# Performance work log

Measured on AMD Instinct MI355X. Metric: run time of the kernel, lower is better.

The kernel has to match this reference:

```python
import jax, jax.numpy as jnp
import numpy as np
import math

B, S, D_MODEL, H, D_LATENT = 2, 2048, 2048, 16, 512
D_HEAD = D_MODEL // H


def setup_inputs() -> dict:
    key = jax.random.key(0)
    ks = jax.random.split(key, 6)
    s = lambda fan: 1.0 / math.sqrt(fan)
    return {
        "x": jax.random.normal(ks[0], (B, S, D_MODEL), dtype=jnp.float32),
        "W_q": jax.random.normal(ks[1], (D_MODEL, D_MODEL), dtype=jnp.float32) * s(D_MODEL),
        "W_down_kv": jax.random.normal(ks[2], (D_LATENT, D_MODEL), dtype=jnp.float32) * s(D_MODEL),
        "W_up_k": jax.random.normal(ks[3], (H, D_HEAD, D_LATENT), dtype=jnp.float32) * s(D_LATENT),
        "W_up_v": jax.random.normal(ks[4], (H, D_HEAD, D_LATENT), dtype=jnp.float32) * s(D_LATENT),
        "W_o": jax.random.normal(ks[5], (D_MODEL, D_MODEL), dtype=jnp.float32) * s(D_MODEL),
    }


def reference(x, W_q, W_down_kv, W_up_k, W_up_v, W_o):
    b, s_len, d_model = x.shape
    # Q: (B, H, S, Dh)
    Q = (x @ W_q.T).reshape(b, s_len, H, D_HEAD).transpose(0, 2, 1, 3)
    # latent KV: (B, S, d_latent)
    C_kv = x @ W_down_kv.T
    # per-head up-projections fused into one einsum: (B, H, S, Dh)
    K = jnp.einsum("bsl,hdl->bhsd", C_kv, W_up_k)
    V = jnp.einsum("bsl,hdl->bhsd", C_kv, W_up_v)
    scores = jnp.einsum("bhsd,bhtd->bhst", Q, K) / math.sqrt(D_HEAD)
    attn = jax.nn.softmax(scores, axis=-1)  # dropout p=0 / eval -> identity
    out = jnp.einsum("bhst,bhtd->bhsd", attn, V)
    out = out.transpose(0, 2, 1, 3).reshape(b, s_len, H * D_HEAD)
    return out @ W_o.T
```

## Files before the change

kernel.cpp:

```cpp
#include <hip/hip_runtime.h>
#include <hip/hip_bf16.h>

typedef __hip_bfloat16 bf16;
typedef __attribute__((ext_vector_type(8))) short short8v;
typedef __attribute__((ext_vector_type(4))) short short4v;
typedef __attribute__((ext_vector_type(4))) float f32x4;
typedef __attribute__((ext_vector_type(16))) float f32x16;
typedef __attribute__((ext_vector_type(4))) unsigned int uint4v;
typedef unsigned int u32;

#define MFMA_16x16x32(a, b, c) __builtin_amdgcn_mfma_f32_16x16x32_bf16((a), (b), (c), 0, 0, 0)
#define MFMA_32x32x16(a, b, c) __builtin_amdgcn_mfma_f32_32x32x16_bf16((a), (b), (c), 0, 0, 0)

constexpr int Bc = 2, Sc = 2048, DMc = 2048, Hc = 16, DLc = 512, DHc = 128;

__device__ __forceinline__ void gload_lds16(const bf16* g, void* lds) {
  __builtin_amdgcn_global_load_lds(
      (const __attribute__((address_space(1))) void*)g,
      (__attribute__((address_space(3))) void*)lds, 16, 0, 0);
}

__device__ __forceinline__ unsigned short bf16bits(float f) {
  return __builtin_bit_cast(unsigned short, __float2bfloat16(f));
}

struct CvtArgs {
  const float* src[6];
  bf16* dst[6];
  unsigned int cum[6];
  unsigned int total4;
};

__global__ __launch_bounds__(256) void cvt_all_kernel(CvtArgs a)
{
  unsigned int i = blockIdx.x * 256 + threadIdx.x;
  const unsigned int stride = gridDim.x * 256;
  for (; i < a.total4; i += stride) {
    int s = 0;
#pragma unroll
    for (int k = 1; k < 6; ++k) s += (i >= a.cum[k]) ? 1 : 0;
    unsigned int off = (i - a.cum[s]) * 4;
    float4 v = *(const float4*)(a.src[s] + off);
    short4v p;
    p[0] = (short)bf16bits(v.x);
    p[1] = (short)bf16bits(v.y);
    p[2] = (short)bf16bits(v.z);
    p[3] = (short)bf16bits(v.w);
    *(short4v*)(a.dst[s] + off) = p;
  }
}

template<int EPI>
__device__ __forceinline__ void gemm_tile_128(
    const bf16* __restrict__ A, const bf16* __restrict__ BT, void* __restrict__ Cv,
    int K, int ldc, int row0, int col0, bf16* As, bf16* Bs)
{
  const int tid = threadIdx.x;
  const int lane = tid & 63, wid = tid >> 6;
  const int wr = wid >> 1, wc = wid & 1;

  f32x4 acc[4][4] = {};

  const int srow = tid >> 2;
  const int scol = (tid & 3) * 8;
  const bf16* Ag = A + (size_t)(row0 + srow) * K + scol;
  const bf16* Bg = BT + (size_t)(col0 + srow) * K + scol;
  char* AsW = (char*)As + wid * 1024;
  char* BsW = (char*)Bs + wid * 1024;

  const int fr = lane & 15, fk = (lane >> 4) * 8;
  const bf16* aRd = As + (wr * 64 + fr) * 32 + fk;
  const bf16* bRd = Bs + (wc * 64 + fr) * 32 + fk;

  for (int k0 = 0; k0 < K; k0 += 32) {
    gload_lds16(Ag, AsW);
    gload_lds16(Ag + (size_t)64 * K, AsW + 4096);
    gload_lds16(Bg, BsW);
    gload_lds16(Bg + (size_t)64 * K, BsW + 4096);
    Ag += 32; Bg += 32;
    __syncthreads();
    short8v a[4], b[4];
#pragma unroll
    for (int m = 0; m < 4; ++m) a[m] = *(const short8v*)(aRd + m * 16 * 32);
#pragma unroll
    for (int n = 0; n < 4; ++n) b[n] = *(const short8v*)(bRd + n * 16 * 32);
#pragma unroll
    for (int m = 0; m < 4; ++m)
#pragma unroll
      for (int n = 0; n < 4; ++n)
        acc[m][n] = MFMA_16x16x32(a[m], b[n], acc[m][n]);
    __syncthreads();
  }

  const int crow = (lane >> 4) * 4, ccol = lane & 15;
  if (EPI == 0) {
    bf16* C = (bf16*)Cv;
#pragma unroll
    for (int m = 0; m < 4; ++m)
#pragma unroll
      for (int n = 0; n < 4; ++n) {
        bf16* Cp = C + (size_t)(row0 + wr * 64 + m * 16 + crow) * ldc
                     + col0 + wc * 64 + n * 16 + ccol;
#pragma unroll
        for (int r = 0; r < 4; ++r)
          Cp[(size_t)r * ldc] = __float2bfloat16(acc[m][n][r]);
      }
  } else if (EPI == 1) {
    bf16* C = (bf16*)Cv;
#pragma unroll
    for (int m = 0; m < 4; ++m)
#pragma unroll
      for (int n = 0; n < 4; ++n) {
        short4v pk;
#pragma unroll
        for (int r = 0; r < 4; ++r)
          pk[r] = (short)bf16bits(acc[m][n][r]);
        bf16* Cp = C + (size_t)(col0 + wc * 64 + n * 16 + ccol) * ldc
                     + row0 + wr * 64 + m * 16 + crow;
        *(short4v*)Cp = pk;
      }
  } else {
    float* C = (float*)Cv;
#pragma unroll
    for (int m = 0; m < 4; ++m)
#pragma unroll
      for (int n = 0; n < 4; ++n) {
        float* Cp = C + (size_t)(row0 + wr * 64 + m * 16 + crow) * ldc
                      + col0 + wc * 64 + n * 16 + ccol;
#pragma unroll
        for (int r = 0; r < 4; ++r)
          Cp[(size_t)r * ldc] = acc[m][n][r];
      }
  }
}

__device__ __forceinline__ int2 xcd_remap(int nx, int ny) {
  int flat = blockIdx.x + nx * blockIdx.y;
  int chunk = (nx * ny) >> 3;
  int role = (flat & 7) * chunk + (flat >> 3);
  return make_int2(role % nx, role / nx);
}

template<int EPI>
__global__ __launch_bounds__(256) void gemm_bt_kernel(
    const bf16* __restrict__ A, const bf16* __restrict__ BT, void* __restrict__ C,
    int K, int N)
{
  __shared__ bf16 As[128 * 32];
  __shared__ bf16 Bs[128 * 32];
  int2 bb = xcd_remap(gridDim.x, gridDim.y);
  gemm_tile_128<EPI>(A, BT, C, K, N, bb.y * 128, bb.x * 128, As, Bs);
}

__global__ __launch_bounds__(256) void qkv_gemm_kernel(
    const bf16* __restrict__ xb, const bf16* __restrict__ Wqb,
    const bf16* __restrict__ Wdkvb, bf16* __restrict__ Qb, bf16* __restrict__ Ck)
{
  __shared__ bf16 As[128 * 32];
  __shared__ bf16 Bs[128 * 32];
  int2 bb = xcd_remap(20, 32);
  const int bx = bb.x, row0 = bb.y * 128;
  if (bx < 16)
    gemm_tile_128<0>(xb, Wqb, Qb, DMc, DMc, row0, bx * 128, As, Bs);
  else
    gemm_tile_128<0>(xb, Wdkvb, Ck, DMc, DLc, row0, (bx - 16) * 128, As, Bs);
}

__global__ __launch_bounds__(256) void up_gemm_kernel(
    const bf16* __restrict__ Ck, const bf16* __restrict__ Wukb,
    const bf16* __restrict__ Wuvb, bf16* __restrict__ Kcat, bf16* __restrict__ VTcat)
{
  __shared__ bf16 As[128 * 32];
  __shared__ bf16 Bs[128 * 32];
  int2 bb = xcd_remap(32, 32);
  const int bx = bb.x, row0 = bb.y * 128;
  if (bx < 16)
    gemm_tile_128<0>(Ck, Wukb, Kcat, DLc, DMc, row0, bx * 128, As, Bs);
  else
    gemm_tile_128<1>(Ck, Wuvb, VTcat, DLc, Bc * Sc, row0, (bx - 16) * 128, As, Bs);
}

constexpr int KVB = 64;
constexpr int NTT = Sc / KVB;
constexpr int VSTR = Bc * Sc;

__global__ __launch_bounds__(256, 2) void mla_attn_kernel(
    const bf16* __restrict__ Q, const bf16* __restrict__ Kcat,
    const bf16* __restrict__ VTcat, bf16* __restrict__ O)
{
  __shared__ bf16 Ks[2][KVB * 128];
  __shared__ bf16 Vs[2][64 * 128];

  const int tid = threadIdx.x, lane = tid & 63, wid = tid >> 6;
  const int l31 = lane & 31, hi = lane >> 5;

  const int flat = blockIdx.x + 16 * (blockIdx.y + 16 * blockIdx.z);
  const int role = (flat & 7) * 64 + (flat >> 3);
  const int qb = role & 15, h = (role >> 4) & 15, b = role >> 8;
  const int q0 = qb * 128 + wid * 32;

  const bf16* Qp = Q + (size_t)(b * Sc + q0 + l31) * DMc + h * DHc + hi * 8;
  short8v qf[8];
#pragma unroll
  for (int kk = 0; kk < 8; ++kk) qf[kk] = *(const short8v*)(Qp + kk * 16);

  const bf16* Kb = Kcat + (size_t)b * Sc * DMc + h * DHc;
  const bf16* Vb = VTcat + (size_t)(h * DHc) * VSTR + b * Sc;

  const int srow = wid * 4 + (lane >> 4);
  const int scolB = (lane & 15) * 16;
  const int swzK0 = ((srow & 7) << 4) ^ (((srow >> 3) & 1) << 6);
  const bf16* kpE = Kb + (size_t)srow * DMc + (((scolB ^ swzK0) & 255) >> 1);
  const bf16* kpO = Kb + (size_t)srow * DMc + ((((scolB ^ swzK0) ^ 128) & 255) >> 1);
  const int swzV0 = ((srow & 7) << 4) ^ (((srow >> 3) & 1) << 7);
  const int vcp = scolB ^ swzV0;
  const bf16* vp = Vb + (size_t)(2 * srow + (vcp >> 7)) * VSTR + ((vcp & 127) >> 1);

  auto STAGE = [&](int buf, int t0) {
    char* kd = (char*)(&Ks[buf][0]) + wid * 1024;
    gload_lds16(kpE + (size_t)t0 * DMc, kd);
    gload_lds16(kpO + (size_t)(t0 + 16) * DMc, kd + 4096);
    gload_lds16(kpE + (size_t)(t0 + 32) * DMc, kd + 8192);
    gload_lds16(kpO + (size_t)(t0 + 48) * DMc, kd + 12288);
    char* vd = (char*)(&Vs[buf][0]) + wid * 1024;
    const bf16* v0 = vp + t0;
    gload_lds16(v0, vd);
    gload_lds16(v0 + (size_t)32 * VSTR, vd + 4096);
    gload_lds16(v0 + (size_t)64 * VSTR, vd + 8192);
    gload_lds16(v0 + (size_t)96 * VSTR, vd + 12288);
  };

  const int swzR = ((l31 & 7) << 4) ^ (((l31 >> 3) & 1) << 6) ^ (((l31 >> 4) & 1) << 7);
  const int swzVR = (((l31 >> 1) & 7) << 4) ^ (((l31 >> 4) & 1) << 7);

  f32x16 oacc[4] = {};
  float m_r = -1e30f, l_r = 0.f, msc = 0.f;
  const float SCL2 = 0.12751650f;
  const float THRraw = 47.0f;

  STAGE(0, 0);
  int cur = 0;

  for (int it = 0; it < NTT; ++it) {
    asm volatile("s_waitcnt vmcnt(0)" ::: "memory");
    __builtin_amdgcn_s_barrier();
    asm volatile("" ::: "memory");
    if (it + 1 < NTT) STAGE(cur ^ 1, (it + 1) * KVB);
    asm volatile("" ::: "memory");

    f32x16 s0 = {}, s1 = {};
    const char* Kc = (const char*)(&Ks[cur][0]);
    __builtin_amdgcn_s_setprio(1);
#pragma unroll
    for (int kk = 0; kk < 8; ++kk) {
      const int cb = (kk * 32 + hi * 16) ^ swzR;
      short8v k0 = *(const short8v*)(Kc + l31 * 256 + cb);
      short8v k1 = *(const short8v*)(Kc + (32 + l31) * 256 + cb);
      s0 = MFMA_32x32x16(k0, qf[kk], s0);
      s1 = MFMA_32x32x16(k1, qf[kk], s1);
    }
    __builtin_amdgcn_s_setprio(0);

    float pm = s0[0];
#pragma unroll
    for (int i = 1; i < 16; ++i) pm = fmaxf(pm, s0[i]);
#pragma unroll
    for (int i = 0; i < 16; ++i) pm = fmaxf(pm, s1[i]);

    if (!__all(pm - m_r <= THRraw)) {
      float red = fmaxf(pm, __shfl_xor(pm, 32, 64));
      float mnew = fmaxf(m_r, red);
      float c = exp2f((m_r - mnew) * SCL2);
      m_r = mnew;
      msc = mnew * SCL2;
      l_r *= c;
#pragma unroll
      for (int db = 0; db < 4; ++db) oacc[db] *= c;
    }

    short8v pf[4];
#pragma unroll
    for (int tt = 0; tt < 2; ++tt) {
      const f32x16& s = tt ? s1 : s0;
#pragma unroll
      for (int half = 0; half < 2; ++half) {
        float e0 = exp2f(__builtin_fmaf(s[half * 8 + 0], SCL2, -msc));
        float e1 = exp2f(__builtin_fmaf(s[half * 8 + 1], SCL2, -msc));
        float e2 = exp2f(__builtin_fmaf(s[half * 8 + 2], SCL2, -msc));
        float e3 = exp2f(__builtin_fmaf(s[half * 8 + 3], SCL2, -msc));
        float e4 = exp2f(__builtin_fmaf(s[half * 8 + 4], SCL2, -msc));
        float e5 = exp2f(__builtin_fmaf(s[half * 8 + 5], SCL2, -msc));
        float e6 = exp2f(__builtin_fmaf(s[half * 8 + 6], SCL2, -msc));
        float e7 = exp2f(__builtin_fmaf(s[half * 8 + 7], SCL2, -msc));
        l_r += ((e0 + e1) + (e2 + e3)) + ((e4 + e5) + (e6 + e7));
        u32 cA, cB, cC, cD;
        asm("v_cvt_pk_bf16_f32 %0, %1, %2" : "=v"(cA) : "v"(e0), "v"(e1));
        asm("v_cvt_pk_bf16_f32 %0, %1, %2" : "=v"(cB) : "v"(e2), "v"(e3));
        asm("v_cvt_pk_bf16_f32 %0, %1, %2" : "=v"(cC) : "v"(e4), "v"(e5));
        asm("v_cvt_pk_bf16_f32 %0, %1, %2" : "=v"(cD) : "v"(e6), "v"(e7));
        asm volatile("v_permlane32_swap_b32 %0, %1" : "+v"(cA), "+v"(cC));
        asm volatile("v_permlane32_swap_b32 %0, %1" : "+v"(cB), "+v"(cD));
        uint4v w;
        w[0] = cA; w[1] = cB; w[2] = cC; w[3] = cD;
        pf[tt * 2 + half] = __builtin_bit_cast(short8v, w);
      }
    }

    const char* Vc = (const char*)(&Vs[cur][0]);
    __builtin_amdgcn_s_setprio(1);
#pragma unroll
    for (int db = 0; db < 4; ++db) {
      const int vrow = (db * 16 + (l31 >> 1)) * 256;
#pragma unroll
      for (int ts = 0; ts < 4; ++ts) {
        const int cb = ((l31 & 1) * 128 + ts * 32 + hi * 16) ^ swzVR;
        short8v vf = *(const short8v*)(Vc + vrow + cb);
        oacc[db] = MFMA_32x32x16(vf, pf[ts], oacc[db]);
      }
    }
    __builtin_amdgcn_s_setprio(0);

    cur ^= 1;
  }

  float l = l_r + __shfl_xor(l_r, 32, 64);
  float inv = 1.f / l;
  bf16* Op = O + (size_t)(b * Sc + q0 + l31) * DMc + h * DHc + hi * 4;
#pragma unroll
  for (int db = 0; db < 4; ++db) {
#pragma unroll
    for (int rq = 0; rq < 4; ++rq) {
      short4v pk;
#pragma unroll
      for (int r = 0; r < 4; ++r)
        pk[r] = (short)bf16bits(oacc[db][rq * 4 + r] * inv);
      *(short4v*)(Op + db * 32 + rq * 8) = pk;
    }
  }
}

extern "C" void kernel_launch(void* const* d_in, const int* in_sizes, int n_in,
                              void* d_out, int out_size, void* d_ws, size_t ws_size,
                              hipStream_t stream)
{
  const float* x    = (const float*)d_in[0];
  const float* Wq   = (const float*)d_in[1];
  const float* Wdkv = (const float*)d_in[2];
  const float* Wuk  = (const float*)d_in[3];
  const float* Wuv  = (const float*)d_in[4];
  const float* Wo   = (const float*)d_in[5];
  float* out = (float*)d_out;

  char* ws = (char*)d_ws;
  bf16* Qb    = (bf16*)(ws + 0);
  bf16* Kcat  = (bf16*)(ws + 16777216);
  bf16* VTcat = (bf16*)(ws + 33554432);
  bf16* xb    = (bf16*)(ws + 50331648);
  bf16* AO    = (bf16*)(ws + 50331648);
  bf16* Ck    = (bf16*)(ws + 67108864);
  bf16* Wqb   = (bf16*)(ws + 71303168);
  bf16* Wdkvb = (bf16*)(ws + 79691776);
  bf16* Wukb  = (bf16*)(ws + 81788928);
  bf16* Wuvb  = (bf16*)(ws + 83886080);
  bf16* Wob   = (bf16*)(ws + 85983232);

  dim3 blk(256, 1, 1);

  CvtArgs ca;
  ca.src[0] = x;    ca.dst[0] = xb;
  ca.src[1] = Wq;   ca.dst[1] = Wqb;
  ca.src[2] = Wdkv; ca.dst[2] = Wdkvb;
  ca.src[3] = Wuk;  ca.dst[3] = Wukb;
  ca.src[4] = Wuv;  ca.dst[4] = Wuvb;
  ca.src[5] = Wo;   ca.dst[5] = Wob;
  unsigned int n4[6] = { (unsigned)(Bc * Sc * DMc / 4), (unsigned)(DMc * DMc / 4),
                         (unsigned)(DLc * DMc / 4),     (unsigned)(Hc * DHc * DLc / 4),
                         (unsigned)(Hc * DHc * DLc / 4),(unsigned)(DMc * DMc / 4) };
  unsigned int acc = 0;
  for (int i = 0; i < 6; ++i) { ca.cum[i] = acc; acc += n4[i]; }
  ca.total4 = acc;
  cvt_all_kernel<<<2048, blk, 0, stream>>>(ca);

  qkv_gemm_kernel<<<dim3(20, (Bc * Sc) / 128), blk, 0, stream>>>(xb, Wqb, Wdkvb, Qb, Ck);

  up_gemm_kernel<<<dim3(32, (Bc * Sc) / 128), blk, 0, stream>>>(Ck, Wukb, Wuvb, Kcat, VTcat);

  mla_attn_kernel<<<dim3(Sc / 128, Hc, Bc), dim3(256, 1, 1), 0, stream>>>(
      Qb, Kcat, VTcat, AO);

  gemm_bt_kernel<2><<<dim3(DMc / 128, (Bc * Sc) / 128), blk, 0, stream>>>(AO, Wob, out, DMc, DMc);
}
```

Measured before the change: 239.8 us.

## Replace 128x128 GEMM tiles with double-buffered swizzled 256x256 tiles

```diff
diff --git a/kernel.cpp b/kernel.cpp
--- a/kernel.cpp
+++ b/kernel.cpp
@@ -50,57 +50,103 @@
   }
 }
 
+#define GPHASE(bufv, KK, MH)                                                \
+  do {                                                                      \
+    const char* ap_ = aR + (bufv) * 32768 + (KK) * 8192 + (MH) * 4096;      \
+    const char* bp_ = bR + (bufv) * 32768 + (KK) * 8192;                    \
+    short8v af_[4], bf_[4];                                                 \
+    _Pragma("unroll")                                                       \
+    for (int m4 = 0; m4 < 4; ++m4)                                          \
+      af_[m4] = *(const short8v*)(ap_ + m4 * 1024);                         \
+    _Pragma("unroll")                                                       \
+    for (int n = 0; n < 4; ++n)                                             \
+      bf_[n] = *(const short8v*)(bp_ + n * 1024);                           \
+    __builtin_amdgcn_s_setprio(1);                                          \
+    _Pragma("unroll")                                                       \
+    for (int m4 = 0; m4 < 4; ++m4)                                          \
+      _Pragma("unroll")                                                     \
+      for (int n = 0; n < 4; ++n)                                           \
+        acc[(MH) * 4 + m4][n] =                                             \
+            MFMA_16x16x32(af_[m4], bf_[n], acc[(MH) * 4 + m4][n]);          \
+    __builtin_amdgcn_s_setprio(0);                                          \
+  } while (0)
+
 template<int EPI>
-__device__ __forceinline__ void gemm_tile_128(
+__device__ __forceinline__ void gemm_tile_256(
     const bf16* __restrict__ A, const bf16* __restrict__ BT, void* __restrict__ Cv,
-    int K, int ldc, int row0, int col0, bf16* As, bf16* Bs)
+    int K, int ldc, int row0, int col0, char* AsC, char* BsC)
 {
   const int tid = threadIdx.x;
   const int lane = tid & 63, wid = tid >> 6;
-  const int wr = wid >> 1, wc = wid & 1;
-
-  f32x4 acc[4][4] = {};
+  const int wm = wid >> 2, wn = wid & 3;
+  const int fr = lane & 15, g = lane >> 4;
+
+  f32x4 acc[8][4] = {};
 
   const int srow = tid >> 2;
-  const int scol = (tid & 3) * 8;
-  const bf16* Ag = A + (size_t)(row0 + srow) * K + scol;
-  const bf16* Bg = BT + (size_t)(col0 + srow) * K + scol;
-  char* AsW = (char*)As + wid * 1024;
-  char* BsW = (char*)Bs + wid * 1024;
-
-  const int fr = lane & 15, fk = (lane >> 4) * 8;
-  const bf16* aRd = As + (wr * 64 + fr) * 32 + fk;
-  const bf16* bRd = Bs + (wc * 64 + fr) * 32 + fk;
-
-  for (int k0 = 0; k0 < K; k0 += 32) {
-    gload_lds16(Ag, AsW);
-    gload_lds16(Ag + (size_t)64 * K, AsW + 4096);
-    gload_lds16(Bg, BsW);
-    gload_lds16(Bg + (size_t)64 * K, BsW + 4096);
-    Ag += 32; Bg += 32;
-    __syncthreads();
-    short8v a[4], b[4];
-#pragma unroll
-    for (int m = 0; m < 4; ++m) a[m] = *(const short8v*)(aRd + m * 16 * 32);
-#pragma unroll
-    for (int n = 0; n < 4; ++n) b[n] = *(const short8v*)(bRd + n * 16 * 32);
-#pragma unroll
-    for (int m = 0; m < 4; ++m)
-#pragma unroll
-      for (int n = 0; n < 4; ++n)
-        acc[m][n] = MFMA_16x16x32(a[m], b[n], acc[m][n]);
-    __syncthreads();
-  }
-
-  const int crow = (lane >> 4) * 4, ccol = lane & 15;
+  const int scolS = ((tid & 3) * 16) ^ (((srow >> 1) & 3) << 4);
+  const bf16* sA = A + (size_t)(row0 + srow) * K + (scolS >> 1);
+  const bf16* sB = BT + (size_t)(col0 + srow) * K + (scolS >> 1);
+  char* AsW = AsC + wid * 1024;
+  char* BsW = BsC + wid * 1024;
+
+  auto ISSA = [&](int buf, int h, int kk, int kt) {
+    gload_lds16(sA + (size_t)(h * 128) * K + kt * 64 + kk * 32,
+                AsW + buf * 32768 + h * 16384 + kk * 8192);
+  };
+  auto ISSB = [&](int buf, int h, int kk, int kt) {
+    gload_lds16(sB + (size_t)(h * 128) * K + kt * 64 + kk * 32,
+                BsW + buf * 32768 + h * 16384 + kk * 8192);
+  };
+
+  const int rdLane = fr * 64 + ((g * 16) ^ (((fr >> 1) & 3) << 4));
+  const char* aR = AsC + wm * 16384 + rdLane;
+  const char* bR = BsC + (wn >> 1) * 16384 + (wn & 1) * 4096 + rdLane;
+
+  ISSA(0, 0, 0, 0); ISSA(0, 1, 0, 0); ISSB(0, 0, 0, 0); ISSB(0, 1, 0, 0);
+  ISSA(0, 0, 1, 0); ISSA(0, 1, 1, 0); ISSB(0, 0, 1, 0); ISSB(0, 1, 1, 0);
+
+  const int KT = K >> 6;
+  for (int kt = 0; kt < KT - 1; ++kt) {
+    const int buf = kt & 1, nb = buf ^ 1;
+    asm volatile("s_waitcnt vmcnt(4)" ::: "memory");
+    __builtin_amdgcn_s_barrier();
+    asm volatile("" ::: "memory");
+    ISSA(nb, 0, 0, kt + 1); ISSA(nb, 1, 0, kt + 1);
+    GPHASE(buf, 0, 0);
+    ISSB(nb, 0, 0, kt + 1); ISSB(nb, 1, 0, kt + 1);
+    GPHASE(buf, 0, 1);
+    asm volatile("s_waitcnt vmcnt(4)" ::: "memory");
+    __builtin_amdgcn_s_barrier();
+    asm volatile("" ::: "memory");
+    ISSA(nb, 0, 1, kt + 1); ISSA(nb, 1, 1, kt + 1);
+    GPHASE(buf, 1, 0);
+    ISSB(nb, 0, 1, kt + 1); ISSB(nb, 1, 1, kt + 1);
+    GPHASE(buf, 1, 1);
+  }
+  {
+    const int buf = (KT - 1) & 1;
+    asm volatile("s_waitcnt vmcnt(4)" ::: "memory");
+    __builtin_amdgcn_s_barrier();
+    asm volatile("" ::: "memory");
+    GPHASE(buf, 0, 0);
+    GPHASE(buf, 0, 1);
+    asm volatile("s_waitcnt vmcnt(0)" ::: "memory");
+    __builtin_amdgcn_s_barrier();
+    asm volatile("" ::: "memory");
+    GPHASE(buf, 1, 0);
+    GPHASE(buf, 1, 1);
+  }
+
+  const int crow = g * 4, ccol = fr;
   if (EPI == 0) {
     bf16* C = (bf16*)Cv;
 #pragma unroll
-    for (int m = 0; m < 4; ++m)
+    for (int m = 0; m < 8; ++m)
 #pragma unroll
       for (int n = 0; n < 4; ++n) {
-        bf16* Cp = C + (size_t)(row0 + wr * 64 + m * 16 + crow) * ldc
-                     + col0 + wc * 64 + n * 16 + ccol;
+        bf16* Cp = C + (size_t)(row0 + wm * 128 + m * 16 + crow) * ldc
+                     + col0 + wn * 64 + n * 16 + ccol;
 #pragma unroll
         for (int r = 0; r < 4; ++r)
           Cp[(size_t)r * ldc] = __float2bfloat16(acc[m][n][r]);
@@ -108,25 +154,25 @@
   } else if (EPI == 1) {
     bf16* C = (bf16*)Cv;
 #pragma unroll
-    for (int m = 0; m < 4; ++m)
+    for (int m = 0; m < 8; ++m)
 #pragma unroll
       for (int n = 0; n < 4; ++n) {
         short4v pk;
 #pragma unroll
         for (int r = 0; r < 4; ++r)
           pk[r] = (short)bf16bits(acc[m][n][r]);
-        bf16* Cp = C + (size_t)(col0 + wc * 64 + n * 16 + ccol) * ldc
-                     + row0 + wr * 64 + m * 16 + crow;
+        bf16* Cp = C + (size_t)(col0 + wn * 64 + n * 16 + ccol) * ldc
+                     + row0 + wm * 128 + m * 16 + crow;
         *(short4v*)Cp = pk;
       }
   } else {
     float* C = (float*)Cv;
 #pragma unroll
-    for (int m = 0; m < 4; ++m)
+    for (int m = 0; m < 8; ++m)
 #pragma unroll
       for (int n = 0; n < 4; ++n) {
-        float* Cp = C + (size_t)(row0 + wr * 64 + m * 16 + crow) * ldc
-                      + col0 + wc * 64 + n * 16 + ccol;
+        float* Cp = C + (size_t)(row0 + wm * 128 + m * 16 + crow) * ldc
+                      + col0 + wn * 64 + n * 16 + ccol;
 #pragma unroll
         for (int r = 0; r < 4; ++r)
           Cp[(size_t)r * ldc] = acc[m][n][r];
@@ -134,50 +180,45 @@
   }
 }
 
-__device__ __forceinline__ int2 xcd_remap(int nx, int ny) {
-  int flat = blockIdx.x + nx * blockIdx.y;
-  int chunk = (nx * ny) >> 3;
-  int role = (flat & 7) * chunk + (flat >> 3);
-  return make_int2(role % nx, role / nx);
-}
-
-template<int EPI>
-__global__ __launch_bounds__(256) void gemm_bt_kernel(
-    const bf16* __restrict__ A, const bf16* __restrict__ BT, void* __restrict__ C,
-    int K, int N)
-{
-  __shared__ bf16 As[128 * 32];
-  __shared__ bf16 Bs[128 * 32];
-  int2 bb = xcd_remap(gridDim.x, gridDim.y);
-  gemm_tile_128<EPI>(A, BT, C, K, N, bb.y * 128, bb.x * 128, As, Bs);
-}
-
-__global__ __launch_bounds__(256) void qkv_gemm_kernel(
+__global__ __launch_bounds__(512, 2) void qkv_gemm_kernel(
     const bf16* __restrict__ xb, const bf16* __restrict__ Wqb,
     const bf16* __restrict__ Wdkvb, bf16* __restrict__ Qb, bf16* __restrict__ Ck)
 {
-  __shared__ bf16 As[128 * 32];
-  __shared__ bf16 Bs[128 * 32];
-  int2 bb = xcd_remap(20, 32);
-  const int bx = bb.x, row0 = bb.y * 128;
-  if (bx < 16)
-    gemm_tile_128<0>(xb, Wqb, Qb, DMc, DMc, row0, bx * 128, As, Bs);
+  __shared__ char As[65536];
+  __shared__ char Bs[65536];
+  const int flat = blockIdx.x + 10 * blockIdx.y;
+  const int role = (flat & 7) * 20 + (flat >> 3);
+  const int bx = role % 10, by = role / 10;
+  if (bx < 8)
+    gemm_tile_256<0>(xb, Wqb, Qb, DMc, DMc, by * 256, bx * 256, As, Bs);
   else
-    gemm_tile_128<0>(xb, Wdkvb, Ck, DMc, DLc, row0, (bx - 16) * 128, As, Bs);
-}
-
-__global__ __launch_bounds__(256) void up_gemm_kernel(
+    gemm_tile_256<0>(xb, Wdkvb, Ck, DMc, DLc, by * 256, (bx - 8) * 256, As, Bs);
+}
+
+__global__ __launch_bounds__(512, 2) void up_gemm_kernel(
     const bf16* __restrict__ Ck, const bf16* __restrict__ Wukb,
     const bf16* __restrict__ Wuvb, bf16* __restrict__ Kcat, bf16* __restrict__ VTcat)
 {
-  __shared__ bf16 As[128 * 32];
-  __shared__ bf16 Bs[128 * 32];
-  int2 bb = xcd_remap(32, 32);
-  const int bx = bb.x, row0 = bb.y * 128;
-  if (bx < 16)
-    gemm_tile_128<0>(Ck, Wukb, Kcat, DLc, DMc, row0, bx * 128, As, Bs);
+  __shared__ char As[65536];
+  __shared__ char Bs[65536];
+  const int flat = blockIdx.x + 16 * blockIdx.y;
+  const int role = (flat & 7) * 32 + (flat >> 3);
+  const int bx = role & 15, by = role >> 4;
+  if (bx < 8)
+    gemm_tile_256<0>(Ck, Wukb, Kcat, DLc, DMc, by * 256, bx * 256, As, Bs);
   else
-    gemm_tile_128<1>(Ck, Wuvb, VTcat, DLc, Bc * Sc, row0, (bx - 16) * 128, As, Bs);
+    gemm_tile_256<1>(Ck, Wuvb, VTcat, DLc, Bc * Sc, by * 256, (bx - 8) * 256, As, Bs);
+}
+
+__global__ __launch_bounds__(512, 2) void out_gemm_kernel(
+    const bf16* __restrict__ AO, const bf16* __restrict__ Wob, float* __restrict__ out)
+{
+  __shared__ char As[65536];
+  __shared__ char Bs[65536];
+  const int flat = blockIdx.x + 8 * blockIdx.y;
+  const int role = (flat & 7) * 16 + (flat >> 3);
+  const int bx = role & 7, by = role >> 3;
+  gemm_tile_256<2>(AO, Wob, out, DMc, DMc, by * 256, bx * 256, As, Bs);
 }
 
 constexpr int KVB = 64;
@@ -381,12 +422,12 @@
   ca.total4 = acc;
   cvt_all_kernel<<<2048, blk, 0, stream>>>(ca);
 
-  qkv_gemm_kernel<<<dim3(20, (Bc * Sc) / 128), blk, 0, stream>>>(xb, Wqb, Wdkvb, Qb, Ck);
-
-  up_gemm_kernel<<<dim3(32, (Bc * Sc) / 128), blk, 0, stream>>>(Ck, Wukb, Wuvb, Kcat, VTcat);
+  qkv_gemm_kernel<<<dim3(10, 16), dim3(512, 1, 1), 0, stream>>>(xb, Wqb, Wdkvb, Qb, Ck);
+
+  up_gemm_kernel<<<dim3(16, 16), dim3(512, 1, 1), 0, stream>>>(Ck, Wukb, Wuvb, Kcat, VTcat);
 
   mla_attn_kernel<<<dim3(Sc / 128, Hc, Bc), dim3(256, 1, 1), 0, stream>>>(
       Qb, Kcat, VTcat, AO);
 
-  gemm_bt_kernel<2><<<dim3(DMc / 128, (Bc * Sc) / 128), blk, 0, stream>>>(AO, Wob, out, DMc, DMc);
-}
+  out_gemm_kernel<<<dim3(8, 16), dim3(512, 1, 1), 0, stream>>>(AO, Wob, out);
+}
```

Measured after the change: 274.6 us. 1.15x slower.
